# Optimization experiments

Measured on AMD Instinct MI355X. Metric: run time of the kernel, lower is better.

The kernel has to match this reference:

```python
import jax, jax.numpy as jnp
import numpy as np

LOSS_WEIGHT = 1.0


def setup_inputs() -> dict:
    key = jax.random.key(0)
    k1, k2 = jax.random.split(key)
    source = jax.random.normal(k1, (8, 4096, 3), dtype=jnp.float32)
    target = jax.random.normal(k2, (8, 4096, 3), dtype=jnp.float32)
    return {"source": source, "target": target}


def reference(source, target):
    # Pairwise Euclidean distances via the Gram-matrix identity (same math as torch.cdist):
    # d(i,j)^2 = ||s_i||^2 + ||t_j||^2 - 2 <s_i, t_j>
    s2 = jnp.sum(source * source, axis=-1)  # [B, N]
    t2 = jnp.sum(target * target, axis=-1)  # [B, M]
    cross = jnp.einsum("bnd,bmd->bnm", source, target)  # [B, N, M]
    d2 = s2[:, :, None] + t2[:, None, :] - 2.0 * cross
    dists = jnp.sqrt(jnp.maximum(d2, 0.0))  # [B, N, M]
    term1 = jnp.mean(jnp.min(dists, axis=2), axis=1)  # source -> nearest target
    term2 = jnp.mean(jnp.min(dists, axis=1), axis=1)  # target -> nearest source
    return LOSS_WEIGHT * (jnp.mean(term1) + jnp.mean(term2))
```

## Files before the change

kernel.cpp:

```cpp
#include <hip/hip_runtime.h>

#define BB 8
#define NN 4096
#define BLK 256
#define RPT 4
#define ROWS 128
#define SLICES 8
#define JSL (NN/SLICES)
#define NBLK (2*BB*(NN/ROWS))

__global__ __launch_bounds__(BLK) void cd_main(const float* __restrict__ src,
                                               const float* __restrict__ tgt,
                                               float* __restrict__ partial) {
    __shared__ float4 tl[NN];
    __shared__ float pmin[SLICES * ROWS];
    __shared__ float bsum[4];
    const int dir = blockIdx.z;
    const float* Sp = dir ? tgt : src;
    const float* Tp = dir ? src : tgt;
    const int b   = blockIdx.y;
    const int rt  = blockIdx.x;
    const int tid = threadIdx.x;

    const float* tb = Tp + (size_t)b * NN * 3;
    for (int k = tid; k < NN; k += BLK) {
        float x = tb[3*k], y = tb[3*k+1], z = tb[3*k+2];
        tl[k] = make_float4(x, y, z, 0.5f*(x*x + y*y + z*z));
    }

    const float* sb = Sp + (size_t)b * NN * 3;
    const int sub   = tid & 31;
    const int slice = tid >> 5;
    const int rowBase = rt * ROWS;
    float nx[RPT], ny[RPT], nz[RPT], q[RPT];
#pragma unroll
    for (int r = 0; r < RPT; ++r) {
        int row = rowBase + sub + 32*r;
        float x = sb[3*row], y = sb[3*row+1], z = sb[3*row+2];
        nx[r] = -x; ny[r] = -y; nz[r] = -z;
        q[r] = 0.5f*(x*x + y*y + z*z);
    }
    __syncthreads();

    float m0[RPT], m1[RPT];
#pragma unroll
    for (int r = 0; r < RPT; ++r) { m0[r] = 1.0e30f; m1[r] = 1.0e30f; }

    const float4* tp = tl + slice * JSL;
#pragma unroll 2
    for (int j = 0; j < JSL; j += 2) {
        float4 t0 = tp[j];
        float4 t1 = tp[j+1];
#pragma unroll
        for (int r = 0; r < RPT; ++r) {
            float a0 = fmaf(nx[r], t0.x, fmaf(ny[r], t0.y, fmaf(nz[r], t0.z, t0.w)));
            float a1 = fmaf(nx[r], t1.x, fmaf(ny[r], t1.y, fmaf(nz[r], t1.z, t1.w)));
            m0[r] = fminf(m0[r], a0);
            m1[r] = fminf(m1[r], a1);
        }
    }

#pragma unroll
    for (int r = 0; r < RPT; ++r)
        pmin[slice*ROWS + sub + 32*r] = fminf(m0[r], m1[r]) + q[r];
    __syncthreads();

    float dsum = 0.0f;
    if (tid < ROWS) {
        float v = pmin[tid];
#pragma unroll
        for (int s = 1; s < SLICES; ++s) v = fminf(v, pmin[s*ROWS + tid]);
        v = fmaxf(v, 0.0f);
        dsum = sqrtf(2.0f * v);
    }
#pragma unroll
    for (int o = 32; o > 0; o >>= 1) dsum += __shfl_down(dsum, o, 64);
    if ((tid & 63) == 0) bsum[tid >> 6] = dsum;
    __syncthreads();
    if (tid == 0)
        partial[((size_t)dir*BB + b)*32 + rt] = bsum[0] + bsum[1] + bsum[2] + bsum[3];
}

__global__ __launch_bounds__(512) void cd_final(const float* __restrict__ partial,
                                                float* __restrict__ out) {
    __shared__ float ps[8];
    float v = partial[threadIdx.x];
#pragma unroll
    for (int o = 32; o > 0; o >>= 1) v += __shfl_down(v, o, 64);
    if ((threadIdx.x & 63) == 0) ps[threadIdx.x >> 6] = v;
    __syncthreads();
    if (threadIdx.x == 0) {
        float t = 0.0f;
#pragma unroll
        for (int w = 0; w < 8; ++w) t += ps[w];
        out[0] = t * (1.0f / (float)(BB * NN));
    }
}

extern "C" void kernel_launch(void* const* d_in, const int* in_sizes, int n_in,
                              void* d_out, int out_size, void* d_ws, size_t ws_size,
                              hipStream_t stream) {
    const float* src = (const float*)d_in[0];
    const float* tgt = (const float*)d_in[1];
    float* partial = (float*)d_ws;
    float* out = (float*)d_out;

    dim3 grid(NN/ROWS, BB, 2);
    cd_main<<<grid, BLK, 0, stream>>>(src, tgt, partial);
    cd_final<<<1, 512, 0, stream>>>(partial, out);
}
```

Baseline: 80.60 us.

## Pre-pack points into float4 and stream targets via wave-uniform scalar loads

A new pre-pass kernel packs every source and target point into a global float4 of (x, y, z, half squared norm). The scan kernel then drops the 64 KB LDS staging of targets. Each wave walks its own 1024-target slice with wave-uniform addresses (readfirstlane), so the loads can become scalar broadcast loads, with a software prefetch of the next four points. Each lane now handles 2 rows instead of 4. This removes per-block LDS fill, LDS read traffic and the occupancy limit from the big LDS buffer, at the cost of an extra kernel launch and a small prefetch read past each slice into workspace.

```diff
diff --git a/kernel.cpp b/kernel.cpp
--- a/kernel.cpp
+++ b/kernel.cpp
@@ -3,82 +3,74 @@
 #define BB 8
 #define NN 4096
 #define BLK 256
-#define RPT 4
-#define ROWS 128
-#define SLICES 8
-#define JSL (NN/SLICES)
-#define NBLK (2*BB*(NN/ROWS))
+#define NPTS (2*BB*NN)
+#define JSL 1024
+#define PK_PAD 8
+#define PARTIAL_OFF 0x110000
 
-__global__ __launch_bounds__(BLK) void cd_main(const float* __restrict__ src,
+__global__ __launch_bounds__(BLK) void cd_pack(const float* __restrict__ src,
                                                const float* __restrict__ tgt,
+                                               float4* __restrict__ pk) {
+    int i = blockIdx.x * BLK + threadIdx.x;
+    const float* p = ((i >> 15) ? tgt : src) + 3 * (i & 32767);
+    float x = p[0], y = p[1], z = p[2];
+    pk[i] = make_float4(x, y, z, 0.5f * (x*x + y*y + z*z));
+}
+
+__global__ __launch_bounds__(BLK) void cd_scan(const float4* __restrict__ pk,
                                                float* __restrict__ partial) {
-    __shared__ float4 tl[NN];
-    __shared__ float pmin[SLICES * ROWS];
-    __shared__ float bsum[4];
+    __shared__ float pm[4][128];
+    __shared__ float bs[4];
     const int dir = blockIdx.z;
-    const float* Sp = dir ? tgt : src;
-    const float* Tp = dir ? src : tgt;
     const int b   = blockIdx.y;
     const int rt  = blockIdx.x;
-    const int tid = threadIdx.x;
+    const int tid = threadIdx.x, lane = tid & 63, wave = tid >> 6;
 
-    const float* tb = Tp + (size_t)b * NN * 3;
-    for (int k = tid; k < NN; k += BLK) {
-        float x = tb[3*k], y = tb[3*k+1], z = tb[3*k+2];
-        tl[k] = make_float4(x, y, z, 0.5f*(x*x + y*y + z*z));
+    const float4* S = pk + (dir ? (size_t)BB*NN : 0) + (size_t)b*NN;
+    const float4* T = pk + (dir ? 0 : (size_t)BB*NN) + (size_t)b*NN;
+
+    float4 s0 = S[rt*128 + lane];
+    float4 s1 = S[rt*128 + 64 + lane];
+    float nx0 = -s0.x, ny0 = -s0.y, nz0 = -s0.z, q0 = s0.w;
+    float nx1 = -s1.x, ny1 = -s1.y, nz1 = -s1.z, q1 = s1.w;
+
+    const int jbase = __builtin_amdgcn_readfirstlane(wave * JSL);
+    const float4* Tw = T + jbase;
+
+    float m0 = 1.0e30f, m1 = 1.0e30f;
+    float4 t0 = Tw[0], t1 = Tw[1], t2 = Tw[2], t3 = Tw[3];
+    for (int j = 0; j < JSL; j += 4) {
+        float4 n0 = Tw[j+4], n1 = Tw[j+5], n2 = Tw[j+6], n3 = Tw[j+7];
+        float a00 = fmaf(nx0, t0.x, fmaf(ny0, t0.y, fmaf(nz0, t0.z, t0.w)));
+        float a10 = fmaf(nx1, t0.x, fmaf(ny1, t0.y, fmaf(nz1, t0.z, t0.w)));
+        float a01 = fmaf(nx0, t1.x, fmaf(ny0, t1.y, fmaf(nz0, t1.z, t1.w)));
+        float a11 = fmaf(nx1, t1.x, fmaf(ny1, t1.y, fmaf(nz1, t1.z, t1.w)));
+        float a02 = fmaf(nx0, t2.x, fmaf(ny0, t2.y, fmaf(nz0, t2.z, t2.w)));
+        float a12 = fmaf(nx1, t2.x, fmaf(ny1, t2.y, fmaf(nz1, t2.z, t2.w)));
+        float a03 = fmaf(nx0, t3.x, fmaf(ny0, t3.y, fmaf(nz0, t3.z, t3.w)));
+        float a13 = fmaf(nx1, t3.x, fmaf(ny1, t3.y, fmaf(nz1, t3.z, t3.w)));
+        m0 = fminf(fminf(fminf(m0, a00), a01), fminf(a02, a03));
+        m1 = fminf(fminf(fminf(m1, a10), a11), fminf(a12, a13));
+        t0 = n0; t1 = n1; t2 = n2; t3 = n3;
     }
 
-    const float* sb = Sp + (size_t)b * NN * 3;
-    const int sub   = tid & 31;
-    const int slice = tid >> 5;
-    const int rowBase = rt * ROWS;
-    float nx[RPT], ny[RPT], nz[RPT], q[RPT];
-#pragma unroll
-    for (int r = 0; r < RPT; ++r) {
-        int row = rowBase + sub + 32*r;
-        float x = sb[3*row], y = sb[3*row+1], z = sb[3*row+2];
-        nx[r] = -x; ny[r] = -y; nz[r] = -z;
-        q[r] = 0.5f*(x*x + y*y + z*z);
-    }
+    pm[wave][lane]      = m0 + q0;
+    pm[wave][64 + lane] = m1 + q1;
     __syncthreads();
 
-    float m0[RPT], m1[RPT];
-#pragma unroll
-    for (int r = 0; r < RPT; ++r) { m0[r] = 1.0e30f; m1[r] = 1.0e30f; }
-
-    const float4* tp = tl + slice * JSL;
-#pragma unroll 2
-    for (int j = 0; j < JSL; j += 2) {
-        float4 t0 = tp[j];
-        float4 t1 = tp[j+1];
-#pragma unroll
-        for (int r = 0; r < RPT; ++r) {
-            float a0 = fmaf(nx[r], t0.x, fmaf(ny[r], t0.y, fmaf(nz[r], t0.z, t0.w)));
-            float a1 = fmaf(nx[r], t1.x, fmaf(ny[r], t1.y, fmaf(nz[r], t1.z, t1.w)));
-            m0[r] = fminf(m0[r], a0);
-            m1[r] = fminf(m1[r], a1);
-        }
-    }
-
-#pragma unroll
-    for (int r = 0; r < RPT; ++r)
-        pmin[slice*ROWS + sub + 32*r] = fminf(m0[r], m1[r]) + q[r];
-    __syncthreads();
-
-    float dsum = 0.0f;
-    if (tid < ROWS) {
-        float v = pmin[tid];
-#pragma unroll
-        for (int s = 1; s < SLICES; ++s) v = fminf(v, pmin[s*ROWS + tid]);
+    float d = 0.0f;
+    if (tid < 128) {
+        float v = fminf(fminf(pm[0][tid], pm[1][tid]),
+                        fminf(pm[2][tid], pm[3][tid]));
         v = fmaxf(v, 0.0f);
-        dsum = sqrtf(2.0f * v);
+        d = sqrtf(2.0f * v);
     }
 #pragma unroll
-    for (int o = 32; o > 0; o >>= 1) dsum += __shfl_down(dsum, o, 64);
-    if ((tid & 63) == 0) bsum[tid >> 6] = dsum;
+    for (int o = 32; o > 0; o >>= 1) d += __shfl_down(d, o, 64);
+    if (lane == 0) bs[wave] = d;
     __syncthreads();
     if (tid == 0)
-        partial[((size_t)dir*BB + b)*32 + rt] = bsum[0] + bsum[1] + bsum[2] + bsum[3];
+        partial[((size_t)dir*BB + b)*32 + rt] = bs[0] + bs[1] + bs[2] + bs[3];
 }
 
 __global__ __launch_bounds__(512) void cd_final(const float* __restrict__ partial,
@@ -102,10 +94,12 @@
                               hipStream_t stream) {
     const float* src = (const float*)d_in[0];
     const float* tgt = (const float*)d_in[1];
-    float* partial = (float*)d_ws;
+    float4* pk = (float4*)d_ws;
+    float* partial = (float*)((char*)d_ws + PARTIAL_OFF);
     float* out = (float*)d_out;
 
-    dim3 grid(NN/ROWS, BB, 2);
-    cd_main<<<grid, BLK, 0, stream>>>(src, tgt, partial);
+    cd_pack<<<NPTS / BLK, BLK, 0, stream>>>(src, tgt, pk);
+    dim3 grid(NN / 128, BB, 2);
+    cd_scan<<<grid, BLK, 0, stream>>>(pk, partial);
     cd_final<<<1, 512, 0, stream>>>(partial, out);
 }
```

After: 103.8 us. 28.8% more time.
